# Kernel optimization log

Measured on AMD Instinct MI355X. Metric: run time of the kernel, lower is better.

The kernel has to match this reference:

```python
import jax, jax.numpy as jnp
import numpy as np

B, N, M, K = 2, 16384, 16384, 32
C_IN, C_OUT, KS = 64, 128, 15
RADIUS = 0.1
SIGMA = 0.5 * RADIUS  # module sets self.sigma = sigma * radius


def _generate_kernel_points(num_kpoints: int, radius: float) -> np.ndarray:
    # Fibonacci-sphere placement, matching the torch generate_kernel_points
    if num_kpoints == 1:
        return np.zeros((1, 3), dtype=np.float32)
    pts = np.zeros((num_kpoints, 3), dtype=np.float32)
    golden_angle = np.pi * (3 - np.sqrt(5))
    for i in range(num_kpoints):
        y = 1 - i / float(num_kpoints - 1) * 2
        r_y = np.sqrt(1 - y * y)
        theta = golden_angle * i
        pts[i] = np.array([np.cos(theta) * r_y, y, np.sin(theta) * r_y]) * radius
    return pts


def setup_inputs() -> dict:
    key = jax.random.key(0)
    k1, k2, k3, k4 = jax.random.split(key, 4)
    query_points = jax.random.uniform(k1, (B, N, 3), dtype=jnp.float32)
    support_points = jax.random.uniform(k2, (B, M, 3), dtype=jnp.float32)
    support_features = jax.random.normal(k3, (B, M, C_IN), dtype=jnp.float32)
    neighbor_idx = jax.random.randint(k4, (B, N, K), 0, M)
    kernel_points = jnp.asarray(_generate_kernel_points(KS, RADIUS * 0.8))
    k5 = jax.random.fold_in(key, 5)
    # kaiming-uniform-ish init on flattened (KS*C_IN, C_OUT)
    bound = np.sqrt(1.0 / (KS * C_IN))
    weights = jax.random.uniform(k5, (KS, C_IN, C_OUT), dtype=jnp.float32,
                                 minval=-bound, maxval=bound)
    bias = jnp.zeros((C_OUT,), dtype=jnp.float32)
    return {
        "query_points": query_points,
        "support_points": support_points,
        "support_features": support_features,
        "neighbor_idx": neighbor_idx,
        "kernel_points": kernel_points,
        "weights": weights,
        "bias": bias,
    }


def reference(query_points, support_points, support_features, neighbor_idx,
              kernel_points, weights, bias):
    # Batched gather: support[b, idx[b]] -> [B, N, K, *]
    gather = jax.vmap(lambda feats, idx: feats[idx])
    neighbor_points = gather(support_points, neighbor_idx)      # [B,N,K,3]
    neighbor_features = gather(support_features, neighbor_idx)  # [B,N,K,C_in]

    rel = neighbor_points - query_points[:, :, None, :]          # [B,N,K,3]
    # squared distance to each kernel point: [B,N,K,J]
    sq_dist = jnp.sum((rel[:, :, :, None, :] - kernel_points[None, None, None]) ** 2,
                      axis=-1)
    influences = jnp.exp(-sq_dist / (2 * SIGMA ** 2))
    influences = influences / (influences.sum(axis=-1, keepdims=True) + 1e-6)

    out = jnp.einsum('bnkc,bnkj,jco->bno', neighbor_features, influences, weights)
    return out + bias
```

## Files before the change

kernel.cpp:

```cpp
#include <hip/hip_runtime.h>
#include <hip/hip_bf16.h>


#define NB   16384
#define MB   16384
#define KN   32
#define CIN  64
#define COUT 128
#define KS   15
#define TP   32
#define PROW 2064
#define WFRAG_BYTES 245760u
#define F16_BYTES   (2u * MB * CIN * 2u)

typedef __attribute__((ext_vector_type(8))) short short8;
typedef __attribute__((ext_vector_type(4))) float f32x4;

static __device__ __forceinline__ unsigned int pack2_bf16(float f0, float f1) {
    const unsigned int a = __float_as_uint(f0) + 0x8000u;
    const unsigned int b = __float_as_uint(f1) + 0x8000u;
    return (a >> 16) | (b & 0xffff0000u);
}

static __device__ __forceinline__ unsigned int pack2_bf16_rne(float f0, float f1) {
    unsigned int a = __float_as_uint(f0);
    unsigned int b = __float_as_uint(f1);
    a += 0x7fffu + ((a >> 16) & 1u);
    b += 0x7fffu + ((b >> 16) & 1u);
    return (a >> 16) | (b & 0xffff0000u);
}

static __device__ __forceinline__ unsigned short f32_to_bf16_rne(float x) {
    unsigned int u = __float_as_uint(x);
    u += 0x7fffu + ((u >> 16) & 1u);
    return (unsigned short)(u >> 16);
}

__global__ __launch_bounds__(256)
void prep_kernel(const float* __restrict__ Wg, const float* __restrict__ feats,
                 unsigned short* __restrict__ wf, unsigned int* __restrict__ f16,
                 int do_feats) {
    const int bid = blockIdx.x;
    if (bid < 60) {
        const int tid = bid * 256 + threadIdx.x;
        const int l = tid & 63;
        const int t = (tid >> 6) & 7;
        const int s = tid >> 9;
        const int n  = t * 16 + (l & 15);
        const int kb = s * 32 + (l >> 4) * 8;
        short8 o;
        #pragma unroll
        for (int i = 0; i < 8; ++i)
            o[i] = (short)f32_to_bf16_rne(Wg[(kb + i) * COUT + n]);
        *(short8*)(wf + (size_t)tid * 8) = o;
    } else if (do_feats) {
        const unsigned int t = (unsigned int)(bid - 60) * 256u + threadIdx.x;
        if (t < 2u * MB * CIN / 2u) {
            const float2 v = ((const float2*)feats)[t];
            f16[t] = pack2_bf16_rne(v.x, v.y);
        }
    }
}

template<bool F16>
__global__ __launch_bounds__(512, 4)
void kpconv_mfma(const float* __restrict__ qp,
                 const float* __restrict__ sp,
                 const float* __restrict__ feats,
                 const unsigned short* __restrict__ fbh16,
                 const int* __restrict__ nidx,
                 const float* __restrict__ kp,
                 const unsigned short* __restrict__ wfrag,
                 const float* __restrict__ bias,
                 float* __restrict__ out) {
    __shared__ __align__(16) char sF[TP * PROW];

    const int tid  = threadIdx.x;
    const int lane = tid & 63;
    const int wv   = tid >> 6;
    const int gp_base = blockIdx.x * TP;
    const int b = gp_base >> 14;
    const float*          fbf = feats + (size_t)b * MB * CIN;
    const unsigned short* fbh = fbh16 + (size_t)b * MB * CIN;
    const float*          spb = sp + (size_t)b * MB * 3;

    const int n16  = lane & 15;
    const int quad = lane >> 4;

    const int jc = n16 < 14 ? n16 : 14;
    const float kxj = kp[3 * jc + 0];
    const float kyj = kp[3 * jc + 1];
    const float kzj = kp[3 * jc + 2];

    #pragma unroll 1
    for (int pt = 0; pt < 4; ++pt) {
        const int pl = wv * 4 + pt;
        const int gp = gp_base + pl;

        const int* ip = nidx + (size_t)gp * KN + quad * 8;
        int idxv[8];
        *(int4*)(&idxv[0]) = *(const int4*)(ip);
        *(int4*)(&idxv[4]) = *(const int4*)(ip + 4);

        const float qx = qp[3 * gp + 0];
        const float qy = qp[3 * gp + 1];
        const float qz = qp[3 * gp + 2];
        const float qkx = qx + kxj, qky = qy + kyj, qkz = qz + kzj;

        float e[8];
        #pragma unroll
        for (int i = 0; i < 8; ++i) {
            const float* s3 = spb + (size_t)idxv[i] * 3;
            const float dx = s3[0] - qkx;
            const float dy = s3[1] - qky;
            const float dz = s3[2] - qkz;
            const float d2 = fmaf(dx, dx, fmaf(dy, dy, dz * dz));
            const float ev = __expf(-200.0f * d2);
            e[i] = (n16 < 15) ? ev : 0.0f;
        }

        unsigned int iu[4];
        float en[8];
        #pragma unroll
        for (int i = 0; i < 8; ++i) {
            float s = e[i];
            s += __shfl_xor(s, 1, 16);
            s += __shfl_xor(s, 2, 16);
            s += __shfl_xor(s, 4, 16);
            s += __shfl_xor(s, 8, 16);
            en[i] = e[i] * __builtin_amdgcn_rcpf(s + 1e-6f);
        }
        #pragma unroll
        for (int ih = 0; ih < 4; ++ih)
            iu[ih] = pack2_bf16(en[2 * ih], en[2 * ih + 1]);
        const short8 ifrag = *(const short8*)iu;

        unsigned int fu[4][4];
        #pragma unroll
        for (int ih = 0; ih < 4; ++ih) {
            if (F16) {
                const unsigned short* fr0 = fbh + (size_t)idxv[2 * ih]     * CIN + n16;
                const unsigned short* fr1 = fbh + (size_t)idxv[2 * ih + 1] * CIN + n16;
                #pragma unroll
                for (int t = 0; t < 4; ++t) {
                    const unsigned int lo = fr0[t * 16];
                    const unsigned int hi = fr1[t * 16];
                    fu[t][ih] = lo | (hi << 16);
                }
            } else {
                const float* fr0 = fbf + (size_t)idxv[2 * ih]     * CIN + n16;
                const float* fr1 = fbf + (size_t)idxv[2 * ih + 1] * CIN + n16;
                #pragma unroll
                for (int t = 0; t < 4; ++t)
                    fu[t][ih] = pack2_bf16(fr0[t * 16], fr1[t * 16]);
            }
        }

        #pragma unroll
        for (int t = 0; t < 4; ++t) {
            const short8 ffrag = *(const short8*)(fu[t]);
            f32x4 z = {0.f, 0.f, 0.f, 0.f};
            const f32x4 dd = __builtin_amdgcn_mfma_f32_16x16x32_bf16(ffrag, ifrag, z, 0, 0, 0);
            const unsigned int lo = pack2_bf16(dd[0], dd[1]);
            const unsigned int hi = pack2_bf16(dd[2], dd[3]);
            const int off = pl * PROW + n16 * 128 +
                            ((t * 32 + quad * 8) ^ ((n16 & 7) << 4));
            uint2 v; v.x = lo; v.y = hi;
            *(uint2*)(sF + off) = v;
        }
    }
    __syncthreads();

    const int lm = n16;
    f32x4 acc0 = {0.f, 0.f, 0.f, 0.f};
    f32x4 acc1 = {0.f, 0.f, 0.f, 0.f};
    const char* aBase = sF + lm * PROW;

    #pragma unroll
    for (int s = 0; s < 30; ++s) {
        const int j   = s >> 1;
        const int c0b = (s & 1) * 64 + quad * 16;
        const int off = j * 128 + (c0b ^ ((j & 7) << 4));
        const short8 a0 = *(const short8*)(aBase + off);
        const short8 a1 = *(const short8*)(aBase + 16 * PROW + off);
        const short8 bf = *(const short8*)(wfrag + ((size_t)(s * 8 + wv) * 64 + lane) * 8);
        acc0 = __builtin_amdgcn_mfma_f32_16x16x32_bf16(a0, bf, acc0, 0, 0, 0);
        acc1 = __builtin_amdgcn_mfma_f32_16x16x32_bf16(a1, bf, acc1, 0, 0, 0);
    }

    const float bsv = bias[wv * 16 + lm];
    #pragma unroll
    for (int r = 0; r < 4; ++r) {
        const int pr = quad * 4 + r;
        out[(size_t)(gp_base + pr)      * COUT + wv * 16 + lm] = acc0[r] + bsv;
        out[(size_t)(gp_base + 16 + pr) * COUT + wv * 16 + lm] = acc1[r] + bsv;
    }
}

extern "C" void kernel_launch(void* const* d_in, const int* in_sizes, int n_in,
                              void* d_out, int out_size, void* d_ws, size_t ws_size,
                              hipStream_t stream) {
    const float* qp = (const float*)d_in[0];
    const float* sp = (const float*)d_in[1];
    const float* ft = (const float*)d_in[2];
    const int*   ni = (const int*)d_in[3];
    const float* kp = (const float*)d_in[4];
    const float* wg = (const float*)d_in[5];
    const float* bs = (const float*)d_in[6];
    float* o = (float*)d_out;

    unsigned short* wfrag = (unsigned short*)d_ws;
    unsigned int*   f16   = (unsigned int*)((char*)d_ws + WFRAG_BYTES);
    const int do_feats = (ws_size >= (size_t)WFRAG_BYTES + F16_BYTES) ? 1 : 0;

    const int prep_blocks = do_feats ? (60 + 4096) : 60;
    hipLaunchKernelGGL(prep_kernel, dim3(prep_blocks), dim3(256), 0, stream,
                       wg, ft, wfrag, f16, do_feats);

    if (do_feats) {
        hipLaunchKernelGGL((kpconv_mfma<true>), dim3((2 * NB) / TP), dim3(512), 0, stream,
                           qp, sp, ft, (const unsigned short*)f16, ni, kp, wfrag, bs, o);
    } else {
        hipLaunchKernelGGL((kpconv_mfma<false>), dim3((2 * NB) / TP), dim3(512), 0, stream,
                           qp, sp, ft, (const unsigned short*)f16, ni, kp, wfrag, bs, o);
    }
}
```

Baseline: 112.6 us.

## Repack features and support points for vectorized gathers and prefetch neighbor indices

The prep kernel now writes the bf16 features in a permuted layout, so each lane fetches its four channel values for a neighbor with one 8-byte load and rebuilds the MFMA fragments with byte permutes. Before, this took four scalar 2-byte loads. Support points are padded to float4, so each coordinate gather becomes a single 16-byte load. Neighbor indices for the next point are prefetched one iteration ahead, and all gathers are issued before the exp math. The cost is extra prep work, extra workspace, and higher register use.

After: 111.6 us. About the same (-0.9%).

```diff
diff --git a/kernel.cpp b/kernel.cpp
--- a/kernel.cpp
+++ b/kernel.cpp
@@ -10,8 +10,9 @@
 #define KS   15
 #define TP   32
 #define PROW 2064
-#define WFRAG_BYTES 245760u
-#define F16_BYTES   (2u * MB * CIN * 2u)
+#define WF_BYTES  245760u
+#define FP_BYTES  (2u * MB * CIN * 2u)
+#define SP4_BYTES (2u * MB * 16u)
 
 typedef __attribute__((ext_vector_type(8))) short short8;
 typedef __attribute__((ext_vector_type(4))) float f32x4;
@@ -38,8 +39,9 @@
 
 __global__ __launch_bounds__(256)
 void prep_kernel(const float* __restrict__ Wg, const float* __restrict__ feats,
-                 unsigned short* __restrict__ wf, unsigned int* __restrict__ f16,
-                 int do_feats) {
+                 const float* __restrict__ sp,
+                 unsigned short* __restrict__ wf, unsigned int* __restrict__ fp,
+                 float4* __restrict__ sp4, int full) {
     const int bid = blockIdx.x;
     if (bid < 60) {
         const int tid = bid * 256 + threadIdx.x;
@@ -53,21 +55,33 @@
         for (int i = 0; i < 8; ++i)
             o[i] = (short)f32_to_bf16_rne(Wg[(kb + i) * COUT + n]);
         *(short8*)(wf + (size_t)tid * 8) = o;
-    } else if (do_feats) {
-        const unsigned int t = (unsigned int)(bid - 60) * 256u + threadIdx.x;
-        if (t < 2u * MB * CIN / 2u) {
-            const float2 v = ((const float2*)feats)[t];
-            f16[t] = pack2_bf16_rne(v.x, v.y);
-        }
-    }
-}
-
-template<bool F16>
+    } else if (!full) {
+        return;
+    } else if (bid < 60 + 128) {
+        const int m = (bid - 60) * 256 + threadIdx.x;
+        const float* s3 = sp + 3 * (size_t)m;
+        sp4[m] = make_float4(s3[0], s3[1], s3[2], 0.0f);
+    } else {
+        const unsigned int t = (unsigned int)(bid - 188) * 256u + threadIdx.x;
+        if (t < 2u * MB * 32u) {
+            const int m   = t >> 5;
+            const int p2  = t & 31;
+            const int n16 = p2 >> 1;
+            const int tt  = (p2 & 1) * 2;
+            const float a = feats[(size_t)m * CIN + tt * 16 + n16];
+            const float b = feats[(size_t)m * CIN + (tt + 1) * 16 + n16];
+            fp[t] = pack2_bf16_rne(a, b);
+        }
+    }
+}
+
+template<bool PK>
 __global__ __launch_bounds__(512, 4)
 void kpconv_mfma(const float* __restrict__ qp,
                  const float* __restrict__ sp,
                  const float* __restrict__ feats,
-                 const unsigned short* __restrict__ fbh16,
+                 const unsigned int* __restrict__ fpk,
+                 const float4* __restrict__ sp4,
                  const int* __restrict__ nidx,
                  const float* __restrict__ kp,
                  const unsigned short* __restrict__ wfrag,
@@ -80,9 +94,10 @@
     const int wv   = tid >> 6;
     const int gp_base = blockIdx.x * TP;
     const int b = gp_base >> 14;
-    const float*          fbf = feats + (size_t)b * MB * CIN;
-    const unsigned short* fbh = fbh16 + (size_t)b * MB * CIN;
-    const float*          spb = sp + (size_t)b * MB * 3;
+    const float*        fbf  = feats + (size_t)b * MB * CIN;
+    const unsigned int* fpb  = fpk + (size_t)b * MB * 32;
+    const float4*       sp4b = sp4 + (size_t)b * MB;
+    const float*        spb  = sp + (size_t)b * MB * 3;
 
     const int n16  = lane & 15;
     const int quad = lane >> 4;
@@ -92,15 +107,24 @@
     const float kyj = kp[3 * jc + 1];
     const float kzj = kp[3 * jc + 2];
 
+    const int gp0 = gp_base + wv * 4;
+    const int* ip = nidx + (size_t)gp0 * KN + quad * 8;
+    int4 nx0 = *(const int4*)(ip);
+    int4 nx1 = *(const int4*)(ip + 4);
+
     #pragma unroll 1
     for (int pt = 0; pt < 4; ++pt) {
         const int pl = wv * 4 + pt;
-        const int gp = gp_base + pl;
-
-        const int* ip = nidx + (size_t)gp * KN + quad * 8;
+        const int gp = gp0 + pt;
+
         int idxv[8];
-        *(int4*)(&idxv[0]) = *(const int4*)(ip);
-        *(int4*)(&idxv[4]) = *(const int4*)(ip + 4);
+        *(int4*)(&idxv[0]) = nx0;
+        *(int4*)(&idxv[4]) = nx1;
+        if (pt < 3) {
+            const int* ipn = ip + (pt + 1) * KN;
+            nx0 = *(const int4*)(ipn);
+            nx1 = *(const int4*)(ipn + 4);
+        }
 
         const float qx = qp[3 * gp + 0];
         const float qy = qp[3 * gp + 1];
@@ -108,15 +132,34 @@
         const float qkx = qx + kxj, qky = qy + kyj, qkz = qz + kzj;
 
         float e[8];
-        #pragma unroll
-        for (int i = 0; i < 8; ++i) {
-            const float* s3 = spb + (size_t)idxv[i] * 3;
-            const float dx = s3[0] - qkx;
-            const float dy = s3[1] - qky;
-            const float dz = s3[2] - qkz;
-            const float d2 = fmaf(dx, dx, fmaf(dy, dy, dz * dz));
-            const float ev = __expf(-200.0f * d2);
-            e[i] = (n16 < 15) ? ev : 0.0f;
+        uint2 g[8];
+        if (PK) {
+            float4 s4[8];
+            #pragma unroll
+            for (int i = 0; i < 8; ++i) s4[i] = sp4b[idxv[i]];
+            #pragma unroll
+            for (int i = 0; i < 8; ++i)
+                g[i] = *(const uint2*)(fpb + (size_t)idxv[i] * 32 + n16 * 2);
+            #pragma unroll
+            for (int i = 0; i < 8; ++i) {
+                const float dx = s4[i].x - qkx;
+                const float dy = s4[i].y - qky;
+                const float dz = s4[i].z - qkz;
+                const float d2 = fmaf(dx, dx, fmaf(dy, dy, dz * dz));
+                const float ev = __expf(-200.0f * d2);
+                e[i] = (n16 < 15) ? ev : 0.0f;
+            }
+        } else {
+            #pragma unroll
+            for (int i = 0; i < 8; ++i) {
+                const float* s3 = spb + (size_t)idxv[i] * 3;
+                const float dx = s3[0] - qkx;
+                const float dy = s3[1] - qky;
+                const float dz = s3[2] - qkz;
+                const float d2 = fmaf(dx, dx, fmaf(dy, dy, dz * dz));
+                const float ev = __expf(-200.0f * d2);
+                e[i] = (n16 < 15) ? ev : 0.0f;
+            }
         }
 
         unsigned int iu[4];
@@ -136,18 +179,19 @@
         const short8 ifrag = *(const short8*)iu;
 
         unsigned int fu[4][4];
-        #pragma unroll
-        for (int ih = 0; ih < 4; ++ih) {
-            if (F16) {
-                const unsigned short* fr0 = fbh + (size_t)idxv[2 * ih]     * CIN + n16;
-                const unsigned short* fr1 = fbh + (size_t)idxv[2 * ih + 1] * CIN + n16;
-                #pragma unroll
-                for (int t = 0; t < 4; ++t) {
-                    const unsigned int lo = fr0[t * 16];
-                    const unsigned int hi = fr1[t * 16];
-                    fu[t][ih] = lo | (hi << 16);
-                }
-            } else {
+        if (PK) {
+            #pragma unroll
+            for (int ih = 0; ih < 4; ++ih) {
+                const unsigned int ax = g[2 * ih].x, bx = g[2 * ih + 1].x;
+                const unsigned int ay = g[2 * ih].y, by = g[2 * ih + 1].y;
+                fu[0][ih] = __builtin_amdgcn_perm(bx, ax, 0x05040100u);
+                fu[1][ih] = __builtin_amdgcn_perm(bx, ax, 0x07060302u);
+                fu[2][ih] = __builtin_amdgcn_perm(by, ay, 0x05040100u);
+                fu[3][ih] = __builtin_amdgcn_perm(by, ay, 0x07060302u);
+            }
+        } else {
+            #pragma unroll
+            for (int ih = 0; ih < 4; ++ih) {
                 const float* fr0 = fbf + (size_t)idxv[2 * ih]     * CIN + n16;
                 const float* fr1 = fbf + (size_t)idxv[2 * ih + 1] * CIN + n16;
                 #pragma unroll
@@ -210,18 +254,19 @@
     float* o = (float*)d_out;
 
     unsigned short* wfrag = (unsigned short*)d_ws;
-    unsigned int*   f16   = (unsigned int*)((char*)d_ws + WFRAG_BYTES);
-    const int do_feats = (ws_size >= (size_t)WFRAG_BYTES + F16_BYTES) ? 1 : 0;
-
-    const int prep_blocks = do_feats ? (60 + 4096) : 60;
+    unsigned int*   fpk   = (unsigned int*)((char*)d_ws + WF_BYTES);
+    float4*         sp4   = (float4*)((char*)d_ws + WF_BYTES + FP_BYTES);
+    const int full = (ws_size >= (size_t)(WF_BYTES + FP_BYTES + SP4_BYTES)) ? 1 : 0;
+
+    const int prep_blocks = full ? (60 + 128 + 4096) : 60;
     hipLaunchKernelGGL(prep_kernel, dim3(prep_blocks), dim3(256), 0, stream,
-                       wg, ft, wfrag, f16, do_feats);
-
-    if (do_feats) {
+                       wg, ft, sp, wfrag, fpk, sp4, full);
+
+    if (full) {
         hipLaunchKernelGGL((kpconv_mfma<true>), dim3((2 * NB) / TP), dim3(512), 0, stream,
-                           qp, sp, ft, (const unsigned short*)f16, ni, kp, wfrag, bs, o);
+                           qp, sp, ft, fpk, sp4, ni, kp, wfrag, bs, o);
     } else {
         hipLaunchKernelGGL((kpconv_mfma<false>), dim3((2 * NB) / TP), dim3(512), 0, stream,
-                           qp, sp, ft, (const unsigned short*)f16, ni, kp, wfrag, bs, o);
-    }
-}
+                           qp, sp, ft, fpk, sp4, ni, kp, wfrag, bs, o);
+    }
+}
```
